# Performance work log

Measured on AMD Instinct MI355X. Metric: run time of the kernel, lower is better.

The kernel has to match this reference:

```python
import jax, jax.numpy as jnp
import numpy as np

DIM = 1024
ATT_DIM = 1024
N_HEADS = 16
HEAD_DIM = ATT_DIM // N_HEADS


def q_rsqrt_np(x):
    # Quake fast inverse sqrt with one Newton iteration, as in the source.
    y = np.asarray([x], dtype=np.float32)
    x2 = y * np.float32(0.5)
    i = y.view(np.int32)
    i = np.right_shift(i, 1)
    i = np.int32(1597463007) - i
    y = i.view(np.float32)
    y = y * (np.float32(1.5) - x2 * y * y)
    # module casts to half: self.scaling = q_rsqrt(head_dim).half()
    return float(np.float16(y[0]))

SCALING = q_rsqrt_np(HEAD_DIM)


def own_softmax(x):
    # max in fp32, exp in fp32, cast exp to fp16, sum in fp16, divide -> fp16
    maxes = jnp.max(x, axis=-1, keepdims=True)
    x_exp = jnp.exp(x - maxes).astype(jnp.float16)
    x_exp_sum = jnp.sum(x_exp, axis=-1, keepdims=True)
    return x_exp / x_exp_sum


def setup_inputs() -> dict:
    key = jax.random.key(0)
    k1, k2, k3 = jax.random.split(key, 3)
    tgt_len = 2048
    x = jax.random.normal(k1, (tgt_len, DIM), dtype=jnp.float32)
    # nn.Linear weights: [out_features, in_features]
    W_in = jax.random.normal(k2, (3 * ATT_DIM, DIM), dtype=jnp.float32) * (1.0 / np.sqrt(DIM))
    W_out = jax.random.normal(k3, (DIM, ATT_DIM), dtype=jnp.float32) * (1.0 / np.sqrt(ATT_DIM))
    return {"x": x, "W_in": W_in, "W_out": W_out, "tgt_len": tgt_len}


def reference(x, W_in, W_out, tgt_len):
    qkv = x @ W_in.T  # [N, 3*att_dim]
    q, k, v = jnp.split(qkv, 3, axis=-1)
    # [N, H, D] -> [H, N, D]
    q = q.reshape(tgt_len, N_HEADS, HEAD_DIM).transpose(1, 0, 2)
    k = k.reshape(tgt_len, N_HEADS, HEAD_DIM).transpose(1, 0, 2)
    v = v.reshape(tgt_len, N_HEADS, HEAD_DIM).transpose(1, 0, 2)
    scores = jnp.einsum('hnd,hmd->hnm', q, k) * SCALING  # [H, N, N] fp32
    probs = own_softmax(scores)  # fp16
    ctx = jnp.einsum('hnm,hmd->hnd', probs.astype(jnp.float32), v)  # [H, N, D]
    ctx = ctx.transpose(1, 0, 2).reshape(tgt_len, ATT_DIM)
    return ctx @ W_out.T
```

## Files before the change

### kernel.cpp

```cpp
#include <hip/hip_runtime.h>
#include <cstring>
#include <cstdint>

#define TGT 2048
#define NH 16
#define HD 64
#define DIM 1024
#define OD3 3072

typedef _Float16 f16x8 __attribute__((ext_vector_type(8)));
typedef _Float16 f16x4 __attribute__((ext_vector_type(4)));
typedef _Float16 f16x2 __attribute__((ext_vector_type(2)));
typedef float f32x4 __attribute__((ext_vector_type(4)));

__device__ __forceinline__ void gload16(const void* g, void* l) {
  __builtin_amdgcn_global_load_lds(
      (const __attribute__((address_space(1))) unsigned int*)g,
      (__attribute__((address_space(3))) unsigned int*)l, 16, 0, 0);
}

__global__ void cast_all(const float* __restrict__ x, const float* __restrict__ win,
                         const float* __restrict__ wout, _Float16* __restrict__ xh,
                         _Float16* __restrict__ winh, _Float16* __restrict__ wouth) {
  const int NX = TGT * DIM / 8, NW = OD3 * DIM / 8, NO = DIM * DIM / 8;
  int i = blockIdx.x * blockDim.x + threadIdx.x;
  const float* src;
  _Float16* dst;
  int off;
  if (i < NX) { src = x; dst = xh; off = i; }
  else if (i < NX + NW) { src = win; dst = winh; off = i - NX; }
  else if (i < NX + NW + NO) { src = wout; dst = wouth; off = i - NX - NW; }
  else return;
  const float4* p = (const float4*)(src + (size_t)off * 8);
  float4 a = p[0], b = p[1];
  f16x8 o;
  o[0] = (_Float16)a.x; o[1] = (_Float16)a.y; o[2] = (_Float16)a.z; o[3] = (_Float16)a.w;
  o[4] = (_Float16)b.x; o[5] = (_Float16)b.y; o[6] = (_Float16)b.z; o[7] = (_Float16)b.w;
  *(f16x8*)(dst + (size_t)off * 8) = o;
}

__global__ __launch_bounds__(256, 3) void gemm_qkv(
    const _Float16* __restrict__ A, const _Float16* __restrict__ B,
    _Float16* __restrict__ qh, _Float16* __restrict__ kg, _Float16* __restrict__ vg) {
  __shared__ __attribute__((aligned(16))) _Float16 As[2][2048];
  __shared__ __attribute__((aligned(16))) _Float16 Bs[2][4096];
  const int tid = threadIdx.x, lane = tid & 63, w = tid >> 6;
  const int g = lane >> 4, c = lane & 15;
  const int wr = w >> 1, wc = w & 1;
  const int id = blockIdx.x;
  const int xcd = id & 7, r = id >> 3;
  const int bm = (r / 3) * 64;
  const int bn = (xcd * 3 + (r % 3)) * 128;
  f32x4 acc[2][4] = {};

#define QKV_STAGE(buf, k0)                                                              \
  {                                                                                     \
    gload16(A + (size_t)(bm + (tid & 63)) * DIM + (k0) + (tid >> 6) * 8,                \
            &As[buf][tid * 8]);                                                         \
    _Pragma("unroll") for (int t = 0; t < 2; ++t) {                                     \
      int e = t * 256 + tid;                                                            \
      gload16(B + (size_t)(bn + (e & 127)) * DIM + (k0) + (e >> 7) * 8,                 \
              &Bs[buf][e * 8]);                                                         \
    }                                                                                   \
  }

  QKV_STAGE(0, 0);
  __syncthreads();
  for (int kk = 0; kk < 32; ++kk) {
    const int cur = kk & 1;
    if (kk + 1 < 32) QKV_STAGE(cur ^ 1, (kk + 1) * 32);
    f16x8 af[2], bf[4];
#pragma unroll
    for (int m = 0; m < 2; ++m) af[m] = *(const f16x8*)(&As[cur][g * 512 + (wr * 32 + m * 16 + c) * 8]);
#pragma unroll
    for (int n = 0; n < 4; ++n) bf[n] = *(const f16x8*)(&Bs[cur][g * 1024 + (wc * 64 + n * 16 + c) * 8]);
    __builtin_amdgcn_s_setprio(1);
#pragma unroll
    for (int m = 0; m < 2; ++m)
#pragma unroll
      for (int n = 0; n < 4; ++n)
        acc[m][n] = __builtin_amdgcn_mfma_f32_16x16x32_f16(af[m], bf[n], acc[m][n], 0, 0, 0);
    __builtin_amdgcn_s_setprio(0);
    __syncthreads();
  }
#undef QKV_STAGE

  const int which = bn >> 10;
  const int bnn = bn & 1023;
  if (which == 0) {
#pragma unroll
    for (int m = 0; m < 2; ++m)
#pragma unroll
      for (int n = 0; n < 4; ++n)
#pragma unroll
        for (int j = 0; j < 4; ++j) {
          int row = bm + wr * 32 + m * 16 + g * 4 + j;
          int o = bnn + wc * 64 + n * 16 + c;
          qh[((size_t)(o >> 6) * TGT + row) * HD + (o & 63)] = (_Float16)acc[m][n][j];
        }
  } else if (which == 1) {
#pragma unroll
    for (int m = 0; m < 2; ++m)
#pragma unroll
      for (int n = 0; n < 4; ++n)
#pragma unroll
        for (int j = 0; j < 4; ++j) {
          int krow = bm + wr * 32 + m * 16 + g * 4 + j;
          int o = bnn + wc * 64 + n * 16 + c;
          int hh = o >> 6, d = o & 63;
          int kt = krow >> 6, rr = krow & 63;
          int blk = (rr >> 4) * 2 + (d >> 5);
          int ln = (rr & 15) + 16 * ((d >> 3) & 3);
          kg[(size_t)hh * 131072 + kt * 4096 + (blk * 64 + ln) * 8 + (d & 7)] =
              (_Float16)acc[m][n][j];
        }
  } else {
#pragma unroll
    for (int m = 0; m < 2; ++m)
#pragma unroll
      for (int n = 0; n < 4; ++n) {
        int krow0 = bm + wr * 32 + m * 16 + g * 4;
        int o = bnn + wc * 64 + n * 16 + c;
        int hh = o >> 6, d = o & 63;
        int kt = krow0 >> 6, k = krow0 & 63;
        int np = d >> 4, cc = d & 15;
        int ks2 = k >> 5, gg = (k >> 2) & 3, e0 = 4 * ((k >> 4) & 1);
        f16x4 v;
#pragma unroll
        for (int j = 0; j < 4; ++j) v[j] = (_Float16)acc[m][n][j];
        *(f16x4*)(vg + (size_t)hh * 131072 + kt * 4096 +
                  ((np * 2 + ks2) * 64 + cc + 16 * gg) * 8 + e0) = v;
      }
  }
}

__global__ __launch_bounds__(256, 2) void gemm_out(
    const _Float16* __restrict__ A, const _Float16* __restrict__ B, float* __restrict__ out) {
  __shared__ __attribute__((aligned(16))) _Float16 As[2][2048];
  __shared__ __attribute__((aligned(16))) _Float16 Bs[2][2048];
  const int tid = threadIdx.x, lane = tid & 63, w = tid >> 6;
  const int g = lane >> 4, c = lane & 15;
  const int wr = w >> 1, wc = w & 1;
  const int id = blockIdx.x;
  const int xcd = id & 7, r = id >> 3;
  const int bm = (r / 2) * 64;
  const int bn = (xcd * 2 + (r % 2)) * 64;
  f32x4 acc[2][2] = {};

#define OUT_STAGE(buf, k0)                                                              \
  {                                                                                     \
    gload16(A + (size_t)(bm + (tid & 63)) * DIM + (k0) + (tid >> 6) * 8,                \
            &As[buf][tid * 8]);                                                         \
    gload16(B + (size_t)(bn + (tid & 63)) * DIM + (k0) + (tid >> 6) * 8,                \
            &Bs[buf][tid * 8]);                                                         \
  }

  OUT_STAGE(0, 0);
  __syncthreads();
  for (int kk = 0; kk < 32; ++kk) {
    const int cur = kk & 1;
    if (kk + 1 < 32) OUT_STAGE(cur ^ 1, (kk + 1) * 32);
    f16x8 af[2], bf[2];
#pragma unroll
    for (int m = 0; m < 2; ++m) af[m] = *(const f16x8*)(&As[cur][g * 512 + (wr * 32 + m * 16 + c) * 8]);
#pragma unroll
    for (int n = 0; n < 2; ++n) bf[n] = *(const f16x8*)(&Bs[cur][g * 512 + (wc * 32 + n * 16 + c) * 8]);
    __builtin_amdgcn_s_setprio(1);
#pragma unroll
    for (int m = 0; m < 2; ++m)
#pragma unroll
      for (int n = 0; n < 2; ++n)
        acc[m][n] = __builtin_amdgcn_mfma_f32_16x16x32_f16(af[m], bf[n], acc[m][n], 0, 0, 0);
    __builtin_amdgcn_s_setprio(0);
    __syncthreads();
  }
#undef OUT_STAGE

#pragma unroll
  for (int m = 0; m < 2; ++m)
#pragma unroll
    for (int n = 0; n < 2; ++n)
#pragma unroll
      for (int j = 0; j < 4; ++j) {
        int row = bm + wr * 32 + m * 16 + g * 4 + j;
        int o = bn + wc * 32 + n * 16 + c;
        out[(size_t)row * DIM + o] = acc[m][n][j];
      }
}

__global__ __launch_bounds__(256, 4) void attn(
    const _Float16* __restrict__ qh, const _Float16* __restrict__ kg,
    const _Float16* __restrict__ vg, float* __restrict__ po, float* __restrict__ pml,
    float scal2) {
  __shared__ __attribute__((aligned(16))) _Float16 Ks[2][4096];
  __shared__ __attribute__((aligned(16))) _Float16 Vs[2][4096];
  const int tid = threadIdx.x, lane = tid & 63, w = tid >> 6;
  const int g = lane >> 4, c = lane & 15;
  const int h = blockIdx.y, qblk = blockIdx.x, ks0 = blockIdx.z;
  const int qrow = qblk * 64 + w * 16 + c;
  const _Float16* kb = kg + (size_t)h * 131072 + (size_t)ks0 * 65536;
  const _Float16* vb = vg + (size_t)h * 131072 + (size_t)ks0 * 65536;

  f16x8 qf[2];
#pragma unroll
  for (int ks = 0; ks < 2; ++ks)
    qf[ks] = *(const f16x8*)(qh + ((size_t)h * TGT + qrow) * HD + ks * 32 + g * 8);

  float m2 = -INFINITY, lsum = 0.f;
  f32x4 oacc[4] = {};

#define ATTN_STAGE(buf, kt)                                                    \
  {                                                                            \
    _Pragma("unroll") for (int t = 0; t < 2; ++t) {                            \
      int chunk = t * 256 + tid;                                               \
      gload16(kb + (size_t)(kt) * 4096 + chunk * 8, &Ks[buf][chunk * 8]);      \
      gload16(vb + (size_t)(kt) * 4096 + chunk * 8, &Vs[buf][chunk * 8]);      \
    }                                                                          \
  }

  ATTN_STAGE(0, 0);
  __syncthreads();

  for (int kt = 0; kt < 16; ++kt) {
    const int cur = kt & 1;
    if (kt + 1 < 16) ATTN_STAGE(cur ^ 1, kt + 1);

    f32x4 s[4] = {};
    __builtin_amdgcn_s_setprio(1);
#pragma unroll
    for (int n = 0; n < 4; ++n)
#pragma unroll
      for (int ks = 0; ks < 2; ++ks) {
        f16x8 kf = *(const f16x8*)(&Ks[cur][((n * 2 + ks) * 64 + lane) * 8]);
        s[n] = __builtin_amdgcn_mfma_f32_16x16x32_f16(kf, qf[ks], s[n], 0, 0, 0);
      }
    __builtin_amdgcn_s_setprio(0);

    f32x4 m4;
#pragma unroll
    for (int j = 0; j < 4; ++j) m4[j] = fmaxf(fmaxf(s[0][j], s[1][j]), fmaxf(s[2][j], s[3][j]));
    float mx = fmaxf(fmaxf(m4[0], m4[1]), fmaxf(m4[2], m4[3]));
    mx = fmaxf(mx, __shfl_xor(mx, 16));
    mx = fmaxf(mx, __shfl_xor(mx, 32));
    float pmax = mx * scal2;

    if (!__all(pmax <= m2 + 8.f)) {
      float mnew = fmaxf(m2, pmax);
      float alpha = __builtin_amdgcn_exp2f(m2 - mnew);
      m2 = mnew;
      lsum *= alpha;
#pragma unroll
      for (int np = 0; np < 4; ++np)
#pragma unroll
        for (int j = 0; j < 4; ++j) oacc[np][j] *= alpha;
    }

    float tsum = 0.f;
    uint32_t pk[4][2];
#pragma unroll
    for (int n = 0; n < 4; ++n) {
      float p0 = __builtin_amdgcn_exp2f(__builtin_fmaf(s[n][0], scal2, -m2));
      float p1 = __builtin_amdgcn_exp2f(__builtin_fmaf(s[n][1], scal2, -m2));
      float p2 = __builtin_amdgcn_exp2f(__builtin_fmaf(s[n][2], scal2, -m2));
      float p3 = __builtin_amdgcn_exp2f(__builtin_fmaf(s[n][3], scal2, -m2));
      tsum += (p0 + p1) + (p2 + p3);
      auto a = __builtin_amdgcn_cvt_pkrtz(p0, p1);
      auto b = __builtin_amdgcn_cvt_pkrtz(p2, p3);
      memcpy(&pk[n][0], &a, 4);
      memcpy(&pk[n][1], &b, 4);
    }
    tsum += __shfl_xor(tsum, 16);
    tsum += __shfl_xor(tsum, 32);
    lsum += tsum;

#pragma unroll
    for (int ks = 0; ks < 2; ++ks) {
      f16x8 pa;
      memcpy(&pa, &pk[2 * ks][0], 16);
      __builtin_amdgcn_s_setprio(1);
#pragma unroll
      for (int np = 0; np < 4; ++np) {
        f16x8 vbf = *(const f16x8*)(&Vs[cur][((np * 2 + ks) * 64 + lane) * 8]);
        oacc[np] = __builtin_amdgcn_mfma_f32_16x16x32_f16(vbf, pa, oacc[np], 0, 0, 0);
      }
      __builtin_amdgcn_s_setprio(0);
    }
    __syncthreads();
  }
#undef ATTN_STAGE

  const size_t pbase = ((((size_t)ks0 * 16 + h) * 32 + qblk) * 64 + (w * 16 + c)) * 64;
#pragma unroll
  for (int np = 0; np < 4; ++np)
    *(f32x4*)(po + pbase + np * 16 + g * 4) = oacc[np];
  if (g == 0) {
    const size_t sbase = ((((size_t)ks0 * 16 + h) * 32 + qblk) * 64 + (w * 16 + c)) * 2;
    pml[sbase] = m2;
    pml[sbase + 1] = lsum;
  }
}

__global__ void attn_combine(const float* __restrict__ po, const float* __restrict__ pml,
                             _Float16* __restrict__ ctxh) {
  int i = blockIdx.x * blockDim.x + threadIdx.x;
  int dq = i & 3, hq = i >> 2;
  int h = hq & 15, q = hq >> 4;
  int qblk = q >> 6, qr = q & 63;
  size_t s0 = ((((size_t)0 * 16 + h) * 32 + qblk) * 64 + qr) * 2;
  size_t s1 = ((((size_t)1 * 16 + h) * 32 + qblk) * 64 + qr) * 2;
  float m0 = pml[s0], l0 = pml[s0 + 1];
  float m1 = pml[s1], l1 = pml[s1 + 1];
  float m = fmaxf(m0, m1);
  float e0 = __builtin_amdgcn_exp2f(m0 - m);
  float e1 = __builtin_amdgcn_exp2f(m1 - m);
  float inv = 1.0f / (l0 * e0 + l1 * e1);
  size_t o0b = ((((size_t)0 * 16 + h) * 32 + qblk) * 64 + qr) * 64 + dq * 16;
  size_t o1b = ((((size_t)1 * 16 + h) * 32 + qblk) * 64 + qr) * 64 + dq * 16;
  f16x8 o2[2];
#pragma unroll
  for (int t = 0; t < 2; ++t) {
    f32x4 a0 = *(const f32x4*)(po + o0b + t * 8);
    f32x4 a4 = *(const f32x4*)(po + o0b + t * 8 + 4);
    f32x4 b0 = *(const f32x4*)(po + o1b + t * 8);
    f32x4 b4 = *(const f32x4*)(po + o1b + t * 8 + 4);
#pragma unroll
    for (int j = 0; j < 4; ++j) {
      o2[t][j] = (_Float16)((a0[j] * e0 + b0[j] * e1) * inv);
      o2[t][j + 4] = (_Float16)((a4[j] * e0 + b4[j] * e1) * inv);
    }
  }
  _Float16* dst = ctxh + (size_t)q * DIM + h * HD + dq * 16;
  *(f16x8*)(dst) = o2[0];
  *(f16x8*)(dst + 8) = o2[1];
}

static float fp16_round_host(float x) {
  uint32_t u; memcpy(&u, &x, 4);
  uint32_t sign = u & 0x80000000u;
  uint32_t exp = (u >> 23) & 0xff;
  uint32_t m = u & 0x7fffffu;
  uint32_t low = m & 0x1fffu, hi = m >> 13;
  if (low > 0x1000u || (low == 0x1000u && (hi & 1))) hi++;
  if (hi == 0x400u) { hi = 0; exp++; }
  uint32_t r = sign | (exp << 23) | (hi << 13);
  float f; memcpy(&f, &r, 4); return f;
}

extern "C" void kernel_launch(void* const* d_in, const int* in_sizes, int n_in,
                              void* d_out, int out_size, void* d_ws, size_t ws_size,
                              hipStream_t stream) {
  const float* x = (const float*)d_in[0];
  const float* Win = (const float*)d_in[1];
  const float* Wout = (const float*)d_in[2];
  float* out = (float*)d_out;
  char* ws = (char*)d_ws;
  _Float16* xh    = (_Float16*)(ws);
  _Float16* winh  = (_Float16*)(ws + (4ull << 20));
  _Float16* wouth = (_Float16*)(ws + (10ull << 20));
  _Float16* qh    = (_Float16*)(ws + (12ull << 20));
  _Float16* kg    = (_Float16*)(ws + (16ull << 20));
  _Float16* vg    = (_Float16*)(ws + (20ull << 20));
  _Float16* ctxh  = (_Float16*)(ws + (24ull << 20));
  float*    po    = (float*)(ws + (28ull << 20));
  float*    pml   = (float*)(ws + (46ull << 20));

  float y = 64.0f;
  volatile float x2 = 32.0f;
  int ib; memcpy(&ib, &y, 4);
  ib = 1597463007 - (ib >> 1);
  memcpy(&y, &ib, 4);
  volatile float t1 = x2 * y;
  volatile float t2 = t1 * y;
  volatile float t3 = 1.5f - t2;
  y = y * t3;
  const float scaling = fp16_round_host(y);
  const float scal2 = scaling * 1.4426950408889634f;

  const int ncast = (TGT * DIM + OD3 * DIM + DIM * DIM) / 8;
  cast_all<<<(ncast + 255) / 256, 256, 0, stream>>>(x, Win, Wout, xh, winh, wouth);
  gemm_qkv<<<768, 256, 0, stream>>>(xh, winh, qh, kg, vg);
  attn<<<dim3(32, NH, 2), 256, 0, stream>>>(qh, kg, vg, po, pml, scal2);
  attn_combine<<<512, 256, 0, stream>>>(po, pml, ctxh);
  gemm_out<<<512, 256, 0, stream>>>(ctxh, wouth, out);
}
```

Measured before the change: 106.6 us.

## Halve M tile in QKV and output GEMMs and relayout LDS staging

Both projection GEMMs shrink the M tile from 64 to 32 rows, doubling the grid (1536 and 1024 blocks), and raise the launch-bounds occupancy hints. The LDS staging layout is rearranged so each wave reads its MFMA fragment as one contiguous 64-lane block, and the warps are now split only along N. The aim is more blocks and waves to fill the GPU's compute units and better hide latency. The cost is less data reuse per block, more global/L2 traffic for the B operand, and fewer MFMAs per synchronisation.

```diff
diff --git a/kernel.cpp b/kernel.cpp
--- a/kernel.cpp
+++ b/kernel.cpp
@@ -39,28 +39,29 @@
   *(f16x8*)(dst + (size_t)off * 8) = o;
 }
 
-__global__ __launch_bounds__(256, 3) void gemm_qkv(
+__global__ __launch_bounds__(256, 6) void gemm_qkv(
     const _Float16* __restrict__ A, const _Float16* __restrict__ B,
     _Float16* __restrict__ qh, _Float16* __restrict__ kg, _Float16* __restrict__ vg) {
-  __shared__ __attribute__((aligned(16))) _Float16 As[2][2048];
+  __shared__ __attribute__((aligned(16))) _Float16 As[2][1024];
   __shared__ __attribute__((aligned(16))) _Float16 Bs[2][4096];
   const int tid = threadIdx.x, lane = tid & 63, w = tid >> 6;
   const int g = lane >> 4, c = lane & 15;
-  const int wr = w >> 1, wc = w & 1;
   const int id = blockIdx.x;
   const int xcd = id & 7, r = id >> 3;
-  const int bm = (r / 3) * 64;
+  const int bm = (r / 3) * 32;
   const int bn = (xcd * 3 + (r % 3)) * 128;
-  f32x4 acc[2][4] = {};
+  f32x4 acc[2][2] = {};
 
 #define QKV_STAGE(buf, k0)                                                              \
   {                                                                                     \
-    gload16(A + (size_t)(bm + (tid & 63)) * DIM + (k0) + (tid >> 6) * 8,                \
-            &As[buf][tid * 8]);                                                         \
+    if (tid < 128) {                                                                    \
+      int row = bm + ((tid >> 6) << 4) + (tid & 15);                                    \
+      gload16(A + (size_t)row * DIM + (k0) + ((tid >> 4) & 3) * 8, &As[buf][tid * 8]);  \
+    }                                                                                   \
     _Pragma("unroll") for (int t = 0; t < 2; ++t) {                                     \
       int e = t * 256 + tid;                                                            \
-      gload16(B + (size_t)(bn + (e & 127)) * DIM + (k0) + (e >> 7) * 8,                 \
-              &Bs[buf][e * 8]);                                                         \
+      int col = bn + ((e >> 7) << 5) + (((e >> 6) & 1) << 4) + (e & 15);                \
+      gload16(B + (size_t)col * DIM + (k0) + ((e >> 4) & 3) * 8, &Bs[buf][e * 8]);      \
     }                                                                                   \
   }
 
@@ -69,16 +70,16 @@
   for (int kk = 0; kk < 32; ++kk) {
     const int cur = kk & 1;
     if (kk + 1 < 32) QKV_STAGE(cur ^ 1, (kk + 1) * 32);
-    f16x8 af[2], bf[4];
-#pragma unroll
-    for (int m = 0; m < 2; ++m) af[m] = *(const f16x8*)(&As[cur][g * 512 + (wr * 32 + m * 16 + c) * 8]);
-#pragma unroll
-    for (int n = 0; n < 4; ++n) bf[n] = *(const f16x8*)(&Bs[cur][g * 1024 + (wc * 64 + n * 16 + c) * 8]);
+    f16x8 af[2], bf[2];
+#pragma unroll
+    for (int m = 0; m < 2; ++m) af[m] = *(const f16x8*)(&As[cur][(m * 64 + lane) * 8]);
+#pragma unroll
+    for (int n = 0; n < 2; ++n) bf[n] = *(const f16x8*)(&Bs[cur][((w * 2 + n) * 64 + lane) * 8]);
     __builtin_amdgcn_s_setprio(1);
 #pragma unroll
     for (int m = 0; m < 2; ++m)
 #pragma unroll
-      for (int n = 0; n < 4; ++n)
+      for (int n = 0; n < 2; ++n)
         acc[m][n] = __builtin_amdgcn_mfma_f32_16x16x32_f16(af[m], bf[n], acc[m][n], 0, 0, 0);
     __builtin_amdgcn_s_setprio(0);
     __syncthreads();
@@ -91,22 +92,22 @@
 #pragma unroll
     for (int m = 0; m < 2; ++m)
 #pragma unroll
-      for (int n = 0; n < 4; ++n)
+      for (int n = 0; n < 2; ++n)
 #pragma unroll
         for (int j = 0; j < 4; ++j) {
-          int row = bm + wr * 32 + m * 16 + g * 4 + j;
-          int o = bnn + wc * 64 + n * 16 + c;
+          int row = bm + m * 16 + g * 4 + j;
+          int o = bnn + w * 32 + n * 16 + c;
           qh[((size_t)(o >> 6) * TGT + row) * HD + (o & 63)] = (_Float16)acc[m][n][j];
         }
   } else if (which == 1) {
 #pragma unroll
     for (int m = 0; m < 2; ++m)
 #pragma unroll
-      for (int n = 0; n < 4; ++n)
+      for (int n = 0; n < 2; ++n)
 #pragma unroll
         for (int j = 0; j < 4; ++j) {
-          int krow = bm + wr * 32 + m * 16 + g * 4 + j;
-          int o = bnn + wc * 64 + n * 16 + c;
+          int krow = bm + m * 16 + g * 4 + j;
+          int o = bnn + w * 32 + n * 16 + c;
           int hh = o >> 6, d = o & 63;
           int kt = krow >> 6, rr = krow & 63;
           int blk = (rr >> 4) * 2 + (d >> 5);
@@ -118,9 +119,9 @@
 #pragma unroll
     for (int m = 0; m < 2; ++m)
 #pragma unroll
-      for (int n = 0; n < 4; ++n) {
-        int krow0 = bm + wr * 32 + m * 16 + g * 4;
-        int o = bnn + wc * 64 + n * 16 + c;
+      for (int n = 0; n < 2; ++n) {
+        int krow0 = bm + m * 16 + g * 4;
+        int o = bnn + w * 32 + n * 16 + c;
         int hh = o >> 6, d = o & 63;
         int kt = krow0 >> 6, k = krow0 & 63;
         int np = d >> 4, cc = d & 15;
@@ -134,25 +135,28 @@
   }
 }
 
-__global__ __launch_bounds__(256, 2) void gemm_out(
+__global__ __launch_bounds__(256, 4) void gemm_out(
     const _Float16* __restrict__ A, const _Float16* __restrict__ B, float* __restrict__ out) {
-  __shared__ __attribute__((aligned(16))) _Float16 As[2][2048];
+  __shared__ __attribute__((aligned(16))) _Float16 As[2][1024];
   __shared__ __attribute__((aligned(16))) _Float16 Bs[2][2048];
   const int tid = threadIdx.x, lane = tid & 63, w = tid >> 6;
   const int g = lane >> 4, c = lane & 15;
-  const int wr = w >> 1, wc = w & 1;
   const int id = blockIdx.x;
   const int xcd = id & 7, r = id >> 3;
-  const int bm = (r / 2) * 64;
+  const int bm = (r / 2) * 32;
   const int bn = (xcd * 2 + (r % 2)) * 64;
-  f32x4 acc[2][2] = {};
+  f32x4 acc[2] = {};
 
 #define OUT_STAGE(buf, k0)                                                              \
   {                                                                                     \
-    gload16(A + (size_t)(bm + (tid & 63)) * DIM + (k0) + (tid >> 6) * 8,                \
-            &As[buf][tid * 8]);                                                         \
-    gload16(B + (size_t)(bn + (tid & 63)) * DIM + (k0) + (tid >> 6) * 8,                \
-            &Bs[buf][tid * 8]);                                                         \
+    if (tid < 128) {                                                                    \
+      int row = bm + ((tid >> 6) << 4) + (tid & 15);                                    \
+      gload16(A + (size_t)row * DIM + (k0) + ((tid >> 4) & 3) * 8, &As[buf][tid * 8]);  \
+    }                                                                                   \
+    {                                                                                   \
+      int col = bn + ((tid >> 6) << 4) + (tid & 15);                                    \
+      gload16(B + (size_t)col * DIM + (k0) + ((tid >> 4) & 3) * 8, &Bs[buf][tid * 8]);  \
+    }                                                                                   \
   }
 
   OUT_STAGE(0, 0);
@@ -160,17 +164,14 @@
   for (int kk = 0; kk < 32; ++kk) {
     const int cur = kk & 1;
     if (kk + 1 < 32) OUT_STAGE(cur ^ 1, (kk + 1) * 32);
-    f16x8 af[2], bf[2];
-#pragma unroll
-    for (int m = 0; m < 2; ++m) af[m] = *(const f16x8*)(&As[cur][g * 512 + (wr * 32 + m * 16 + c) * 8]);
-#pragma unroll
-    for (int n = 0; n < 2; ++n) bf[n] = *(const f16x8*)(&Bs[cur][g * 512 + (wc * 32 + n * 16 + c) * 8]);
+    f16x8 af[2], bf;
+#pragma unroll
+    for (int m = 0; m < 2; ++m) af[m] = *(const f16x8*)(&As[cur][(m * 64 + lane) * 8]);
+    bf = *(const f16x8*)(&Bs[cur][(w * 64 + lane) * 8]);
     __builtin_amdgcn_s_setprio(1);
 #pragma unroll
     for (int m = 0; m < 2; ++m)
-#pragma unroll
-      for (int n = 0; n < 2; ++n)
-        acc[m][n] = __builtin_amdgcn_mfma_f32_16x16x32_f16(af[m], bf[n], acc[m][n], 0, 0, 0);
+      acc[m] = __builtin_amdgcn_mfma_f32_16x16x32_f16(af[m], bf, acc[m], 0, 0, 0);
     __builtin_amdgcn_s_setprio(0);
     __syncthreads();
   }
@@ -179,13 +180,11 @@
 #pragma unroll
   for (int m = 0; m < 2; ++m)
 #pragma unroll
-    for (int n = 0; n < 2; ++n)
-#pragma unroll
-      for (int j = 0; j < 4; ++j) {
-        int row = bm + wr * 32 + m * 16 + g * 4 + j;
-        int o = bn + wc * 32 + n * 16 + c;
-        out[(size_t)row * DIM + o] = acc[m][n][j];
-      }
+    for (int j = 0; j < 4; ++j) {
+      int row = bm + m * 16 + g * 4 + j;
+      int o = bn + w * 16 + c;
+      out[(size_t)row * DIM + o] = acc[m][j];
+    }
 }
 
 __global__ __launch_bounds__(256, 4) void attn(
@@ -378,8 +377,8 @@
 
   const int ncast = (TGT * DIM + OD3 * DIM + DIM * DIM) / 8;
   cast_all<<<(ncast + 255) / 256, 256, 0, stream>>>(x, Win, Wout, xh, winh, wouth);
-  gemm_qkv<<<768, 256, 0, stream>>>(xh, winh, qh, kg, vg);
+  gemm_qkv<<<1536, 256, 0, stream>>>(xh, winh, qh, kg, vg);
   attn<<<dim3(32, NH, 2), 256, 0, stream>>>(qh, kg, vg, po, pml, scal2);
   attn_combine<<<512, 256, 0, stream>>>(po, pml, ctxh);
-  gemm_out<<<512, 256, 0, stream>>>(ctxh, wouth, out);
-}
+  gemm_out<<<1024, 256, 0, stream>>>(ctxh, wouth, out);
+}
```

New measurement: 128.8 us. +20.9%, slower.

## Fuse split-K attention combine into attention kernel via intra-block LDS merge

Applied to the files above, without the earlier changes.

Each attention block now runs two 256-thread groups, each covering half of the key sequence. Their partial outputs and softmax statistics are merged through LDS, and fp16 context is written directly. This removes the separate combine kernel, one launch, and the fp32 partial-output round trip through global memory. In exchange the block is twice as large with double the LDS footprint, which may lower occupancy. It also relies on the main-loop __syncthreads now spanning both groups.

```diff
diff --git a/kernel.cpp b/kernel.cpp
--- a/kernel.cpp
+++ b/kernel.cpp
@@ -188,18 +188,19 @@
       }
 }
 
-__global__ __launch_bounds__(256, 4) void attn(
+__global__ __launch_bounds__(512, 4) void attn(
     const _Float16* __restrict__ qh, const _Float16* __restrict__ kg,
-    const _Float16* __restrict__ vg, float* __restrict__ po, float* __restrict__ pml,
-    float scal2) {
-  __shared__ __attribute__((aligned(16))) _Float16 Ks[2][4096];
-  __shared__ __attribute__((aligned(16))) _Float16 Vs[2][4096];
-  const int tid = threadIdx.x, lane = tid & 63, w = tid >> 6;
+    const _Float16* __restrict__ vg, _Float16* __restrict__ ctxh, float scal2) {
+  __shared__ __attribute__((aligned(16))) _Float16 Ks[2][2][4096];
+  __shared__ __attribute__((aligned(16))) _Float16 Vs[2][2][4096];
+  const int tid = threadIdx.x;
+  const int grp = tid >> 8, t256 = tid & 255;
+  const int lane = tid & 63, w = (tid >> 6) & 3;
   const int g = lane >> 4, c = lane & 15;
-  const int h = blockIdx.y, qblk = blockIdx.x, ks0 = blockIdx.z;
+  const int h = blockIdx.y, qblk = blockIdx.x;
   const int qrow = qblk * 64 + w * 16 + c;
-  const _Float16* kb = kg + (size_t)h * 131072 + (size_t)ks0 * 65536;
-  const _Float16* vb = vg + (size_t)h * 131072 + (size_t)ks0 * 65536;
+  const _Float16* kb = kg + (size_t)h * 131072 + (size_t)grp * 65536;
+  const _Float16* vb = vg + (size_t)h * 131072 + (size_t)grp * 65536;
 
   f16x8 qf[2];
 #pragma unroll
@@ -209,13 +210,13 @@
   float m2 = -INFINITY, lsum = 0.f;
   f32x4 oacc[4] = {};
 
-#define ATTN_STAGE(buf, kt)                                                    \
-  {                                                                            \
-    _Pragma("unroll") for (int t = 0; t < 2; ++t) {                            \
-      int chunk = t * 256 + tid;                                               \
-      gload16(kb + (size_t)(kt) * 4096 + chunk * 8, &Ks[buf][chunk * 8]);      \
-      gload16(vb + (size_t)(kt) * 4096 + chunk * 8, &Vs[buf][chunk * 8]);      \
-    }                                                                          \
+#define ATTN_STAGE(buf, kt)                                                         \
+  {                                                                                 \
+    _Pragma("unroll") for (int t = 0; t < 2; ++t) {                                 \
+      int chunk = t * 256 + t256;                                                   \
+      gload16(kb + (size_t)(kt) * 4096 + chunk * 8, &Ks[grp][buf][chunk * 8]);      \
+      gload16(vb + (size_t)(kt) * 4096 + chunk * 8, &Vs[grp][buf][chunk * 8]);      \
+    }                                                                               \
   }
 
   ATTN_STAGE(0, 0);
@@ -231,7 +232,7 @@
     for (int n = 0; n < 4; ++n)
 #pragma unroll
       for (int ks = 0; ks < 2; ++ks) {
-        f16x8 kf = *(const f16x8*)(&Ks[cur][((n * 2 + ks) * 64 + lane) * 8]);
+        f16x8 kf = *(const f16x8*)(&Ks[grp][cur][((n * 2 + ks) * 64 + lane) * 8]);
         s[n] = __builtin_amdgcn_mfma_f32_16x16x32_f16(kf, qf[ks], s[n], 0, 0, 0);
       }
     __builtin_amdgcn_s_setprio(0);
@@ -280,7 +281,7 @@
       __builtin_amdgcn_s_setprio(1);
 #pragma unroll
       for (int np = 0; np < 4; ++np) {
-        f16x8 vbf = *(const f16x8*)(&Vs[cur][((np * 2 + ks) * 64 + lane) * 8]);
+        f16x8 vbf = *(const f16x8*)(&Vs[grp][cur][((np * 2 + ks) * 64 + lane) * 8]);
         oacc[np] = __builtin_amdgcn_mfma_f32_16x16x32_f16(vbf, pa, oacc[np], 0, 0, 0);
       }
       __builtin_amdgcn_s_setprio(0);
@@ -289,49 +290,32 @@
   }
 #undef ATTN_STAGE
 
-  const size_t pbase = ((((size_t)ks0 * 16 + h) * 32 + qblk) * 64 + (w * 16 + c)) * 64;
-#pragma unroll
-  for (int np = 0; np < 4; ++np)
-    *(f32x4*)(po + pbase + np * 16 + g * 4) = oacc[np];
-  if (g == 0) {
-    const size_t sbase = ((((size_t)ks0 * 16 + h) * 32 + qblk) * 64 + (w * 16 + c)) * 2;
-    pml[sbase] = m2;
-    pml[sbase + 1] = lsum;
-  }
-}
-
-__global__ void attn_combine(const float* __restrict__ po, const float* __restrict__ pml,
-                             _Float16* __restrict__ ctxh) {
-  int i = blockIdx.x * blockDim.x + threadIdx.x;
-  int dq = i & 3, hq = i >> 2;
-  int h = hq & 15, q = hq >> 4;
-  int qblk = q >> 6, qr = q & 63;
-  size_t s0 = ((((size_t)0 * 16 + h) * 32 + qblk) * 64 + qr) * 2;
-  size_t s1 = ((((size_t)1 * 16 + h) * 32 + qblk) * 64 + qr) * 2;
-  float m0 = pml[s0], l0 = pml[s0 + 1];
-  float m1 = pml[s1], l1 = pml[s1 + 1];
-  float m = fmaxf(m0, m1);
-  float e0 = __builtin_amdgcn_exp2f(m0 - m);
-  float e1 = __builtin_amdgcn_exp2f(m1 - m);
-  float inv = 1.0f / (l0 * e0 + l1 * e1);
-  size_t o0b = ((((size_t)0 * 16 + h) * 32 + qblk) * 64 + qr) * 64 + dq * 16;
-  size_t o1b = ((((size_t)1 * 16 + h) * 32 + qblk) * 64 + qr) * 64 + dq * 16;
-  f16x8 o2[2];
-#pragma unroll
-  for (int t = 0; t < 2; ++t) {
-    f32x4 a0 = *(const f32x4*)(po + o0b + t * 8);
-    f32x4 a4 = *(const f32x4*)(po + o0b + t * 8 + 4);
-    f32x4 b0 = *(const f32x4*)(po + o1b + t * 8);
-    f32x4 b4 = *(const f32x4*)(po + o1b + t * 8 + 4);
-#pragma unroll
-    for (int j = 0; j < 4; ++j) {
-      o2[t][j] = (_Float16)((a0[j] * e0 + b0[j] * e1) * inv);
-      o2[t][j + 4] = (_Float16)((a4[j] * e0 + b4[j] * e1) * inv);
+  float* smo = (float*)&Ks[0][0][0];
+  float* sml = (float*)&Vs[0][0][0];
+  if (grp == 1) {
+#pragma unroll
+    for (int np = 0; np < 4; ++np)
+#pragma unroll
+      for (int j = 0; j < 4; ++j) smo[t256 * 16 + np * 4 + j] = oacc[np][j];
+    sml[t256 * 2] = m2;
+    sml[t256 * 2 + 1] = lsum;
+  }
+  __syncthreads();
+  if (grp == 0) {
+    float m1 = sml[t256 * 2], l1 = sml[t256 * 2 + 1];
+    float mm = fmaxf(m2, m1);
+    float e0 = __builtin_amdgcn_exp2f(m2 - mm);
+    float e1 = __builtin_amdgcn_exp2f(m1 - mm);
+    float inv = 1.0f / (lsum * e0 + l1 * e1);
+#pragma unroll
+    for (int np = 0; np < 4; ++np) {
+      f16x4 o4;
+#pragma unroll
+      for (int j = 0; j < 4; ++j)
+        o4[j] = (_Float16)((oacc[np][j] * e0 + smo[t256 * 16 + np * 4 + j] * e1) * inv);
+      *(f16x4*)(ctxh + (size_t)qrow * DIM + h * HD + np * 16 + g * 4) = o4;
     }
   }
-  _Float16* dst = ctxh + (size_t)q * DIM + h * HD + dq * 16;
-  *(f16x8*)(dst) = o2[0];
-  *(f16x8*)(dst + 8) = o2[1];
 }
 
 static float fp16_round_host(float x) {
@@ -361,8 +345,6 @@
   _Float16* kg    = (_Float16*)(ws + (16ull << 20));
   _Float16* vg    = (_Float16*)(ws + (20ull << 20));
   _Float16* ctxh  = (_Float16*)(ws + (24ull << 20));
-  float*    po    = (float*)(ws + (28ull << 20));
-  float*    pml   = (float*)(ws + (46ull << 20));
 
   float y = 64.0f;
   volatile float x2 = 32.0f;
@@ -379,7 +361,6 @@
   const int ncast = (TGT * DIM + OD3 * DIM + DIM * DIM) / 8;
   cast_all<<<(ncast + 255) / 256, 256, 0, stream>>>(x, Win, Wout, xh, winh, wouth);
   gemm_qkv<<<768, 256, 0, stream>>>(xh, winh, qh, kg, vg);
-  attn<<<dim3(32, NH, 2), 256, 0, stream>>>(qh, kg, vg, po, pml, scal2);
-  attn_combine<<<512, 256, 0, stream>>>(po, pml, ctxh);
+  attn<<<dim3(32, NH), 512, 0, stream>>>(qh, kg, vg, ctxh, scal2);
   gemm_out<<<512, 256, 0, stream>>>(ctxh, wouth, out);
 }
```

Measured after the change: 101.9 us. 4.4% less time.
